# Performance work log

Measured on AMD Instinct MI355X. Metric: run time of the kernel, lower is better.

Reference implementation:

```python
import jax, jax.numpy as jnp
import numpy as np

B, N, M, L, H = 32, 4096, 256, 128, 4
GAMMA = 2.0


def setup_inputs() -> dict:
    key = jax.random.key(0)
    kx, km, kv, ku, kw = jax.random.split(key, 5)
    x = jax.random.normal(kx, (B, N, M), dtype=jnp.float32)
    masks = (jax.random.uniform(km, (B, N)) > 0.3).astype(jnp.float32)
    # VarianceScaling(scale=0.1, fan_in, uniform) ~ small init; exact dist doesn't affect math
    V = jax.random.normal(kv, (H, M, L), dtype=jnp.float32) * 0.02
    U = jax.random.normal(ku, (H, M, L), dtype=jnp.float32) * 0.02
    w = jax.random.normal(kw, (H, L, 1), dtype=jnp.float32) * 0.05
    return {"x": x, "masks": masks, "V": V, "U": U, "w": w}


def reference(x, masks, V, U, w):
    # x: [B,N,M], masks: [B,N], V/U: [H,M,L], w: [H,L,1]
    m = masks[:, None, :, None]  # [B,1,N,1] broadcast over heads
    gated = jnp.tanh(jnp.einsum('bnm,hml->bhnl', x, V)) * jax.nn.sigmoid(
        jnp.einsum('bnm,hml->bhnl', x, U))          # [B,H,N,L]
    logits = jnp.einsum('bhnl,hl->bhn', gated, w[..., 0])[..., None]  # [B,H,N,1]
    a = m * logits                                   # masked logits (as in original)
    a = m * jnp.exp(a)                               # masked exp
    a = a / jnp.sum(a, axis=2, keepdims=True)        # softmax over instances
    ag = a ** GAMMA
    a = ag / jnp.sum(ag, axis=2, keepdims=True)      # gamma-power renorm
    emb = jnp.einsum('bhnk,bnm->bhm', a, x)          # weighted sum; k is the trailing 1
    emb = emb.reshape(B, H * M)                      # concat heads along axis=1
    att = jnp.transpose(a, (1, 0, 2, 3))             # [H,B,N,1] (per-head attention list)
    return (att, emb)
```

## Files before the change

### kernel.cpp

```cpp
#include <hip/hip_runtime.h>
#include <hip/hip_bf16.h>
#include <stdint.h>

#define B_ 32
#define N_ 4096
#define M_ 256
#define L_ 128
#define H_ 4
#define BN_ (B_ * N_)

typedef __bf16 bf16x8 __attribute__((ext_vector_type(8)));
typedef float  f32x4  __attribute__((ext_vector_type(4)));

__device__ __forceinline__ unsigned short f2bf(float f) {
    unsigned int u = __float_as_uint(f);
    u += 0x7fffu + ((u >> 16) & 1u);
    return (unsigned short)(u >> 16);
}
__device__ __forceinline__ unsigned int pack2(float lo, float hi) {
    return (unsigned int)f2bf(lo) | ((unsigned int)f2bf(hi) << 16);
}

__device__ __forceinline__ void gload16(const void* g, void* l) {
    __builtin_amdgcn_global_load_lds(
        (const __attribute__((address_space(1))) unsigned int*)g,
        (__attribute__((address_space(3))) unsigned int*)l, 16, 0, 0);
}


__global__ void prep_x(const float* __restrict__ x, unsigned short* __restrict__ xb) {
    const int blk  = blockIdx.x;
    const int tile = blk >> 2, ks = blk & 3;
    const int i    = threadIdx.x;
    const int kk   = (i & 7) * 8;
    const int tl   = kk >> 5;
    const int kl   = kk & 31;
    char* dst = (char*)xb + ((size_t)tile * 8 + ks * 2 + tl) * 8192;
#pragma unroll
    for (int rep = 0; rep < 4; ++rep) {
        int row = rep * 32 + (i >> 3);
        const float* gx = x + (size_t)(tile * 128 + row) * M_ + ks * 64 + kk;
        float4 a = *(const float4*)gx;
        float4 b = *(const float4*)(gx + 4);
        uint4 o;
        o.x = pack2(a.x, a.y); o.y = pack2(a.z, a.w);
        o.z = pack2(b.x, b.y); o.w = pack2(b.z, b.w);
        int byte = (row * 64 + kl * 2) ^ ((row & 6) << 3);
        *(uint4*)(dst + byte) = o;
    }
}

__global__ void prep_vu_img(const float* __restrict__ V, const float* __restrict__ U,
                            unsigned short* __restrict__ vu) {
    __shared__ float slab[64][129];
    const int b   = blockIdx.x;
    const int mat = b & 1, ks = (b >> 1) & 3, h = b >> 3;
    const float* src = (mat ? U : V) + ((size_t)h * M_ + ks * 64) * L_;
    const int tid = threadIdx.x;
#pragma unroll
    for (int rep = 0; rep < 32; ++rep) {
        int idx = rep * 256 + tid;
        slab[idx >> 7][idx & 127] = src[(size_t)(idx >> 7) * L_ + (idx & 127)];
    }
    __syncthreads();
#pragma unroll
    for (int rep = 0; rep < 4; ++rep) {
        int cidx = rep * 256 + tid;
        int l  = cidx >> 3;
        int kk = (cidx & 7) * 8;
        uint4 o;
        o.x = pack2(slab[kk + 0][l], slab[kk + 1][l]);
        o.y = pack2(slab[kk + 2][l], slab[kk + 3][l]);
        o.z = pack2(slab[kk + 4][l], slab[kk + 5][l]);
        o.w = pack2(slab[kk + 6][l], slab[kk + 7][l]);
        int tl = kk >> 5, kl = kk & 31;
        char* dst = (char*)vu + (((size_t)(h * 8 + ks * 2 + tl)) * 2 + mat) * 8192;
        int byte = (l * 64 + kl * 2) ^ ((l & 6) << 3);
        *(uint4*)(dst + byte) = o;
    }
}

__global__ __launch_bounds__(256, 3)
void gemm_fast5(const unsigned short* __restrict__ xb,
                const unsigned short* __restrict__ vu,
                const float* __restrict__ w,
                float* __restrict__ logits) {
    __shared__ __align__(16) unsigned short xs[2][4096];
    __shared__ __align__(16) unsigned short vs[2][4096];
    __shared__ __align__(16) unsigned short us[2][4096];

    const int orig    = blockIdx.x;
    const int logical = (orig & 7) * 512 + (orig >> 3);
    const int tile    = logical >> 2;
    const int h       = logical & 3;

    const int tid  = threadIdx.x;
    const int lane = tid & 63;
    const int wv   = tid >> 6;
    const int g    = lane >> 4;
    const int c    = lane & 15;

    f32x4 accV[2][8], accU[2][8];
#pragma unroll
    for (int rf = 0; rf < 2; ++rf)
#pragma unroll
        for (int cf = 0; cf < 8; ++cf) {
            accV[rf][cf] = (f32x4){0.f, 0.f, 0.f, 0.f};
            accU[rf][cf] = (f32x4){0.f, 0.f, 0.f, 0.f};
        }

    const int soff = wv * 2048;

    const char* gxs = (const char*)xb + (size_t)tile * 65536 + soff + lane * 16;
    const char* gvs = (const char*)vu + (size_t)h * 131072 + soff + lane * 16;
    const char* gus = gvs + 8192;

    int ar = wv * 32 + c;
    const int aoff0 = (ar * 64 + g * 16) ^ ((ar & 6) << 3);
    const int aoff1 = ((ar + 16) * 64 + g * 16) ^ (((ar + 16) & 6) << 3);
    int boff[8];
#pragma unroll
    for (int cf = 0; cf < 8; ++cf) {
        int l = cf * 16 + c;
        boff[cf] = (l * 64 + g * 16) ^ ((l & 6) << 3);
    }

#define SCHED __builtin_amdgcn_sched_barrier(0)

#define STAGE(t, bufi) do {                                          \
        const char* _gx = gxs + (t) * 8192;                          \
        const char* _gv = gvs + (t) * 16384;                         \
        const char* _gu = gus + (t) * 16384;                         \
        gload16(_gx,        (char*)xs[bufi] + soff);                 \
        gload16(_gx + 1024, (char*)xs[bufi] + soff + 1024);          \
        gload16(_gv,        (char*)vs[bufi] + soff);                 \
        gload16(_gv + 1024, (char*)vs[bufi] + soff + 1024);          \
        gload16(_gu,        (char*)us[bufi] + soff);                 \
        gload16(_gu + 1024, (char*)us[bufi] + soff + 1024);          \
    } while (0)

    STAGE(0, 0);
    SCHED;

#pragma unroll
    for (int t = 0; t < 8; ++t) {
        asm volatile("s_waitcnt vmcnt(0)" ::: "memory");
        __builtin_amdgcn_s_barrier();
        SCHED;

        if (t < 7) STAGE(t + 1, (t + 1) & 1);
        SCHED;

        const int buf = t & 1;
        const char* xbuf = (const char*)xs[buf];
        const char* vbuf = (const char*)vs[buf];
        const char* ubuf = (const char*)us[buf];

        bf16x8 a0 = *(const bf16x8*)(xbuf + aoff0);
        bf16x8 a1 = *(const bf16x8*)(xbuf + aoff1);
        __builtin_amdgcn_s_setprio(1);
#pragma unroll
        for (int cf = 0; cf < 8; ++cf) {
            bf16x8 bv = *(const bf16x8*)(vbuf + boff[cf]);
            bf16x8 bu = *(const bf16x8*)(ubuf + boff[cf]);
            accV[0][cf] = __builtin_amdgcn_mfma_f32_16x16x32_bf16(a0, bv, accV[0][cf], 0, 0, 0);
            accV[1][cf] = __builtin_amdgcn_mfma_f32_16x16x32_bf16(a1, bv, accV[1][cf], 0, 0, 0);
            accU[0][cf] = __builtin_amdgcn_mfma_f32_16x16x32_bf16(a0, bu, accU[0][cf], 0, 0, 0);
            accU[1][cf] = __builtin_amdgcn_mfma_f32_16x16x32_bf16(a1, bu, accU[1][cf], 0, 0, 0);
        }
        __builtin_amdgcn_s_setprio(0);
    }
#undef STAGE
#undef SCHED

    const float* wrow = w + h * L_;
#pragma unroll
    for (int rf = 0; rf < 2; ++rf) {
        float plog[4] = {0.f, 0.f, 0.f, 0.f};
#pragma unroll
        for (int cf = 0; cf < 8; ++cf) {
            float wvv = wrow[cf * 16 + c];
#pragma unroll
            for (int i = 0; i < 4; ++i) {
                float vv = accV[rf][cf][i];
                float uu = accU[rf][cf][i];
                vv = fminf(fmaxf(vv, -20.f), 20.f);
                float A = __expf(2.f * vv);
                float E = __expf(fminf(-uu, 30.f));
                float gg = __fdividef(A - 1.f, (A + 1.f) * (1.f + E));
                plog[i] += gg * wvv;
            }
        }
#pragma unroll
        for (int i = 0; i < 4; ++i) {
            float v = plog[i];
            v += __shfl_xor(v, 1);
            v += __shfl_xor(v, 2);
            v += __shfl_xor(v, 4);
            v += __shfl_xor(v, 8);
            if (c == 0) {
                int rowflat = tile * 128 + wv * 32 + rf * 16 + g * 4 + i;
                int b = rowflat >> 12;
                int n = rowflat & (N_ - 1);
                logits[((size_t)b * H_ + h) * N_ + n] = v;
            }
        }
    }
}

__global__ void prep_vu_slow(const float* __restrict__ V, const float* __restrict__ U,
                             unsigned short* __restrict__ Vt, unsigned short* __restrict__ Ut) {
    int idx = blockIdx.x * 256 + threadIdx.x;
    int m = idx & (M_ - 1);
    int l = (idx >> 8) & (L_ - 1);
    int h = idx >> 15;
    Vt[idx] = f2bf(V[((size_t)h * M_ + m) * L_ + l]);
    Ut[idx] = f2bf(U[((size_t)h * M_ + m) * L_ + l]);
}

#define BM 128
#define BK 64

__global__ __launch_bounds__(256, 2)
void gemm_logits(const float* __restrict__ x,
                 const unsigned short* __restrict__ Vt,
                 const unsigned short* __restrict__ Ut,
                 const float* __restrict__ w,
                 float* __restrict__ logits) {
    __shared__ __align__(16) unsigned short xs[BM * BK];
    __shared__ __align__(16) unsigned short vs[L_ * BK];
    __shared__ __align__(16) unsigned short us[L_ * BK];
    __shared__ float wl[L_];

    const int h    = blockIdx.x >> 10;
    const int tile = blockIdx.x & 1023;
    const int row0 = tile * BM;
    const int tid  = threadIdx.x;
    const int lane = tid & 63;
    const int wave = tid >> 6;

    if (tid < L_) wl[tid] = w[h * L_ + tid];

    f32x4 accV[2][8], accU[2][8];
#pragma unroll
    for (int rf = 0; rf < 2; ++rf)
#pragma unroll
        for (int cf = 0; cf < 8; ++cf) {
            accV[rf][cf] = (f32x4){0.f, 0.f, 0.f, 0.f};
            accU[rf][cf] = (f32x4){0.f, 0.f, 0.f, 0.f};
        }

    const unsigned short* Vh = Vt + (size_t)h * L_ * M_;
    const unsigned short* Uh = Ut + (size_t)h * L_ * M_;
    const int g = lane >> 4;
    const int c = lane & 15;

    for (int ks = 0; ks < 4; ++ks) {
        const int k0 = ks * BK;
        __syncthreads();
#pragma unroll
        for (int p = 0; p < 4; ++p) {
            int row = p * 32 + (tid >> 3);
            int kk  = (tid & 7) * 8;
            const float* gx = x + (size_t)(row0 + row) * M_ + k0 + kk;
            float4 a = *(const float4*)gx;
            float4 b = *(const float4*)(gx + 4);
            uint4 o;
            o.x = pack2(a.x, a.y); o.y = pack2(a.z, a.w);
            o.z = pack2(b.x, b.y); o.w = pack2(b.z, b.w);
            int byte = (row * BK + kk) * 2;
            byte ^= (row & 7) << 4;
            *(uint4*)((char*)xs + byte) = o;
        }
#pragma unroll
        for (int p = 0; p < 4; ++p) {
            int l  = p * 32 + (tid >> 3);
            int kk = (tid & 7) * 8;
            uint4 v = *(const uint4*)(Vh + (size_t)l * M_ + k0 + kk);
            uint4 u = *(const uint4*)(Uh + (size_t)l * M_ + k0 + kk);
            int byte = (l * BK + kk) * 2;
            byte ^= (l & 7) << 4;
            *(uint4*)((char*)vs + byte) = v;
            *(uint4*)((char*)us + byte) = u;
        }
        __syncthreads();
#pragma unroll
        for (int ksub = 0; ksub < 2; ++ksub) {
            bf16x8 afr[2];
#pragma unroll
            for (int rf = 0; rf < 2; ++rf) {
                int row = wave * 32 + rf * 16 + c;
                int byte = (row * BK + ksub * 32 + g * 8) * 2;
                byte ^= (row & 7) << 4;
                afr[rf] = *(const bf16x8*)((const char*)xs + byte);
            }
#pragma unroll
            for (int cf = 0; cf < 8; ++cf) {
                int l = cf * 16 + c;
                int byte = (l * BK + ksub * 32 + g * 8) * 2;
                byte ^= (l & 7) << 4;
                bf16x8 bv = *(const bf16x8*)((const char*)vs + byte);
                bf16x8 bu = *(const bf16x8*)((const char*)us + byte);
#pragma unroll
                for (int rf = 0; rf < 2; ++rf) {
                    accV[rf][cf] = __builtin_amdgcn_mfma_f32_16x16x32_bf16(afr[rf], bv, accV[rf][cf], 0, 0, 0);
                    accU[rf][cf] = __builtin_amdgcn_mfma_f32_16x16x32_bf16(afr[rf], bu, accU[rf][cf], 0, 0, 0);
                }
            }
        }
    }
#pragma unroll
    for (int rf = 0; rf < 2; ++rf) {
        float plog[4] = {0.f, 0.f, 0.f, 0.f};
#pragma unroll
        for (int cf = 0; cf < 8; ++cf) {
            float wvv = wl[cf * 16 + c];
#pragma unroll
            for (int i = 0; i < 4; ++i) {
                float vv = accV[rf][cf][i];
                float uu = accU[rf][cf][i];
                vv = fminf(fmaxf(vv, -20.f), 20.f);
                float e2v = __expf(2.f * vv);
                float t = __fdividef(e2v - 1.f, e2v + 1.f);
                float s = __fdividef(1.f, 1.f + __expf(-uu));
                plog[i] += t * s * wvv;
            }
        }
#pragma unroll
        for (int i = 0; i < 4; ++i) {
            float v = plog[i];
            v += __shfl_xor(v, 1);
            v += __shfl_xor(v, 2);
            v += __shfl_xor(v, 4);
            v += __shfl_xor(v, 8);
            if (c == 0) {
                int rowflat = row0 + wave * 32 + rf * 16 + g * 4 + i;
                int b = rowflat >> 12;
                int n = rowflat & (N_ - 1);
                logits[((size_t)b * H_ + h) * N_ + n] = v;
            }
        }
    }
}

__global__ __launch_bounds__(256)
void softmax_att(const float* __restrict__ logits, const float* __restrict__ masks,
                 float* __restrict__ att) {
    const int bh = blockIdx.x;
    const int b = bh >> 2, h = bh & 3;
    __shared__ float e2s[N_];
    __shared__ float red[4];
    const int tid = threadIdx.x;

    float sum = 0.f;
#pragma unroll
    for (int i = 0; i < N_ / 256; ++i) {
        int n = i * 256 + tid;
        float lg = logits[((size_t)b * H_ + h) * N_ + n];
        float mv = masks[(size_t)b * N_ + n];
        float e = mv * __expf(mv * lg);
        float e2 = e * e;
        e2s[n] = e2;
        sum += e2;
    }
#pragma unroll
    for (int off = 32; off >= 1; off >>= 1) sum += __shfl_xor(sum, off);
    if ((tid & 63) == 0) red[tid >> 6] = sum;
    __syncthreads();
    float S = red[0] + red[1] + red[2] + red[3];
    float inv = 1.f / S;
#pragma unroll
    for (int i = 0; i < N_ / 256; ++i) {
        int n = i * 256 + tid;
        att[((size_t)h * B_ + b) * N_ + n] = e2s[n] * inv;
    }
}

#define NCH 32
#define CHUNK (N_ / NCH)

__global__ __launch_bounds__(256)
void emb_partial(const float* __restrict__ x, const float* __restrict__ att,
                 float* __restrict__ part) {
    const int bc = blockIdx.x;
    const int b = bc >> 5, ch = bc & 31;
    __shared__ float as[H_][CHUNK];
    const int tid = threadIdx.x;

    for (int i = tid; i < H_ * CHUNK; i += 256) {
        int hh = i >> 7;
        int j  = i & (CHUNK - 1);
        as[hh][j] = att[((size_t)hh * B_ + b) * N_ + ch * CHUNK + j];
    }
    __syncthreads();

    float a0 = 0.f, a1 = 0.f, a2 = 0.f, a3 = 0.f;
    const float* xp = x + ((size_t)b * N_ + ch * CHUNK) * M_ + tid;
#pragma unroll 4
    for (int j = 0; j < CHUNK; ++j) {
        float xv = xp[(size_t)j * M_];
        a0 += as[0][j] * xv;
        a1 += as[1][j] * xv;
        a2 += as[2][j] * xv;
        a3 += as[3][j] * xv;
    }
    float* pp = part + (size_t)bc * H_ * M_ + tid;
    pp[0 * M_] = a0; pp[1 * M_] = a1; pp[2 * M_] = a2; pp[3 * M_] = a3;
}

__global__ __launch_bounds__(256)
void emb_reduce(const float* __restrict__ part, float* __restrict__ emb) {
    int idx = blockIdx.x * 256 + threadIdx.x;
    int b = idx >> 10;
    int r = idx & 1023;
    float s = 0.f;
#pragma unroll
    for (int ci = 0; ci < NCH; ++ci)
        s += part[((size_t)(b * NCH + ci)) * (H_ * M_) + r];
    emb[idx] = s;
}

extern "C" void kernel_launch(void* const* d_in, const int* in_sizes, int n_in,
                              void* d_out, int out_size, void* d_ws, size_t ws_size,
                              hipStream_t stream) {
    const float* x     = (const float*)d_in[0];
    const float* masks = (const float*)d_in[1];
    const float* V     = (const float*)d_in[2];
    const float* U     = (const float*)d_in[3];
    const float* w     = (const float*)d_in[4];

    float* att = (float*)d_out;
    float* emb = att + (size_t)H_ * B_ * N_;

    char* ws = (char*)d_ws;
    const size_t XB_BYTES  = (size_t)1024 * 8 * 8192;
    const size_t VU_BYTES  = (size_t)64 * 8192;
    const size_t LG_BYTES  = (size_t)B_ * H_ * N_ * 4;
    const size_t PT_BYTES  = (size_t)B_ * NCH * H_ * M_ * 4;
    const size_t NEED_FAST = XB_BYTES + VU_BYTES + LG_BYTES + PT_BYTES;

    float* logits;
    float* partp;

    if (ws_size >= NEED_FAST) {
        unsigned short* xb = (unsigned short*)ws;
        unsigned short* vuimg = (unsigned short*)(ws + XB_BYTES);
        logits = (float*)(ws + XB_BYTES + VU_BYTES);
        partp  = (float*)(ws + XB_BYTES + VU_BYTES + LG_BYTES);

        prep_x     <<<4096, 256, 0, stream>>>(x, xb);
        prep_vu_img<<<32,   256, 0, stream>>>(V, U, vuimg);
        gemm_fast5 <<<4096, 256, 0, stream>>>(xb, vuimg, w, logits);
    } else {
        unsigned short* Vt = (unsigned short*)ws;
        unsigned short* Ut = (unsigned short*)(ws + 262144);
        logits = (float*)(ws + 524288);
        partp  = (float*)(ws + 524288 + LG_BYTES);

        prep_vu_slow<<<512, 256, 0, stream>>>(V, U, Vt, Ut);
        gemm_logits <<<4096, 256, 0, stream>>>(x, Vt, Ut, w, logits);
    }

    softmax_att<<<B_ * H_,              256, 0, stream>>>(logits, masks, att);
    emb_partial<<<B_ * NCH,             256, 0, stream>>>(x, att, partp);
    emb_reduce <<<(B_ * H_ * M_) / 256, 256, 0, stream>>>(partp, emb);
}
```

Measured before the change: 181.1 us.

## Split GEMM waves into 2x2 row/column grid and widen LDS swizzle

Each wave now computes a 64x64 quadrant (4 row fragments by 4 column fragments) instead of 32 rows by all 128 columns. This balances A and B LDS fragment loads per MFMA, cutting LDS read traffic per wave. Partial logits from the two column halves are combined through a small shared array with an extra barrier. The XOR swizzle is widened from (row&6) to (row&14) in both prep kernels and the GEMM to reduce LDS bank conflicts under the new access pattern.

```diff
diff --git a/kernel.cpp b/kernel.cpp
--- a/kernel.cpp
+++ b/kernel.cpp
@@ -45,7 +45,7 @@
         uint4 o;
         o.x = pack2(a.x, a.y); o.y = pack2(a.z, a.w);
         o.z = pack2(b.x, b.y); o.w = pack2(b.z, b.w);
-        int byte = (row * 64 + kl * 2) ^ ((row & 6) << 3);
+        int byte = (row * 64 + kl * 2) ^ ((row & 14) << 3);
         *(uint4*)(dst + byte) = o;
     }
 }
@@ -75,19 +75,20 @@
         o.w = pack2(slab[kk + 6][l], slab[kk + 7][l]);
         int tl = kk >> 5, kl = kk & 31;
         char* dst = (char*)vu + (((size_t)(h * 8 + ks * 2 + tl)) * 2 + mat) * 8192;
-        int byte = (l * 64 + kl * 2) ^ ((l & 6) << 3);
+        int byte = (l * 64 + kl * 2) ^ ((l & 14) << 3);
         *(uint4*)(dst + byte) = o;
     }
 }
 
 __global__ __launch_bounds__(256, 3)
-void gemm_fast5(const unsigned short* __restrict__ xb,
+void gemm_fast6(const unsigned short* __restrict__ xb,
                 const unsigned short* __restrict__ vu,
                 const float* __restrict__ w,
                 float* __restrict__ logits) {
     __shared__ __align__(16) unsigned short xs[2][4096];
     __shared__ __align__(16) unsigned short vs[2][4096];
     __shared__ __align__(16) unsigned short us[2][4096];
+    __shared__ float part[2][128];
 
     const int orig    = blockIdx.x;
     const int logical = (orig & 7) * 512 + (orig >> 3);
@@ -99,12 +100,14 @@
     const int wv   = tid >> 6;
     const int g    = lane >> 4;
     const int c    = lane & 15;
-
-    f32x4 accV[2][8], accU[2][8];
-#pragma unroll
-    for (int rf = 0; rf < 2; ++rf)
-#pragma unroll
-        for (int cf = 0; cf < 8; ++cf) {
+    const int wr   = wv & 1;
+    const int wc   = wv >> 1;
+
+    f32x4 accV[4][4], accU[4][4];
+#pragma unroll
+    for (int rf = 0; rf < 4; ++rf)
+#pragma unroll
+        for (int cf = 0; cf < 4; ++cf) {
             accV[rf][cf] = (f32x4){0.f, 0.f, 0.f, 0.f};
             accU[rf][cf] = (f32x4){0.f, 0.f, 0.f, 0.f};
         }
@@ -115,14 +118,16 @@
     const char* gvs = (const char*)vu + (size_t)h * 131072 + soff + lane * 16;
     const char* gus = gvs + 8192;
 
-    int ar = wv * 32 + c;
-    const int aoff0 = (ar * 64 + g * 16) ^ ((ar & 6) << 3);
-    const int aoff1 = ((ar + 16) * 64 + g * 16) ^ (((ar + 16) & 6) << 3);
-    int boff[8];
-#pragma unroll
-    for (int cf = 0; cf < 8; ++cf) {
-        int l = cf * 16 + c;
-        boff[cf] = (l * 64 + g * 16) ^ ((l & 6) << 3);
+    int aoff[4], boff[4];
+#pragma unroll
+    for (int rf = 0; rf < 4; ++rf) {
+        int r = wr * 64 + rf * 16 + c;
+        aoff[rf] = (r * 64 + g * 16) ^ ((r & 14) << 3);
+    }
+#pragma unroll
+    for (int cf = 0; cf < 4; ++cf) {
+        int l = wc * 64 + cf * 16 + c;
+        boff[cf] = (l * 64 + g * 16) ^ ((l & 14) << 3);
     }
 
 #define SCHED __builtin_amdgcn_sched_barrier(0)
@@ -156,29 +161,35 @@
         const char* vbuf = (const char*)vs[buf];
         const char* ubuf = (const char*)us[buf];
 
-        bf16x8 a0 = *(const bf16x8*)(xbuf + aoff0);
-        bf16x8 a1 = *(const bf16x8*)(xbuf + aoff1);
+        bf16x8 a0 = *(const bf16x8*)(xbuf + aoff[0]);
+        bf16x8 a1 = *(const bf16x8*)(xbuf + aoff[1]);
+        bf16x8 a2 = *(const bf16x8*)(xbuf + aoff[2]);
+        bf16x8 a3 = *(const bf16x8*)(xbuf + aoff[3]);
         __builtin_amdgcn_s_setprio(1);
 #pragma unroll
-        for (int cf = 0; cf < 8; ++cf) {
+        for (int cf = 0; cf < 4; ++cf) {
             bf16x8 bv = *(const bf16x8*)(vbuf + boff[cf]);
             bf16x8 bu = *(const bf16x8*)(ubuf + boff[cf]);
             accV[0][cf] = __builtin_amdgcn_mfma_f32_16x16x32_bf16(a0, bv, accV[0][cf], 0, 0, 0);
             accV[1][cf] = __builtin_amdgcn_mfma_f32_16x16x32_bf16(a1, bv, accV[1][cf], 0, 0, 0);
+            accV[2][cf] = __builtin_amdgcn_mfma_f32_16x16x32_bf16(a2, bv, accV[2][cf], 0, 0, 0);
+            accV[3][cf] = __builtin_amdgcn_mfma_f32_16x16x32_bf16(a3, bv, accV[3][cf], 0, 0, 0);
             accU[0][cf] = __builtin_amdgcn_mfma_f32_16x16x32_bf16(a0, bu, accU[0][cf], 0, 0, 0);
             accU[1][cf] = __builtin_amdgcn_mfma_f32_16x16x32_bf16(a1, bu, accU[1][cf], 0, 0, 0);
+            accU[2][cf] = __builtin_amdgcn_mfma_f32_16x16x32_bf16(a2, bu, accU[2][cf], 0, 0, 0);
+            accU[3][cf] = __builtin_amdgcn_mfma_f32_16x16x32_bf16(a3, bu, accU[3][cf], 0, 0, 0);
         }
         __builtin_amdgcn_s_setprio(0);
     }
 #undef STAGE
 #undef SCHED
 
-    const float* wrow = w + h * L_;
-#pragma unroll
-    for (int rf = 0; rf < 2; ++rf) {
+    const float* wrow = w + h * L_ + wc * 64;
+#pragma unroll
+    for (int rf = 0; rf < 4; ++rf) {
         float plog[4] = {0.f, 0.f, 0.f, 0.f};
 #pragma unroll
-        for (int cf = 0; cf < 8; ++cf) {
+        for (int cf = 0; cf < 4; ++cf) {
             float wvv = wrow[cf * 16 + c];
 #pragma unroll
             for (int i = 0; i < 4; ++i) {
@@ -198,13 +209,17 @@
             v += __shfl_xor(v, 2);
             v += __shfl_xor(v, 4);
             v += __shfl_xor(v, 8);
-            if (c == 0) {
-                int rowflat = tile * 128 + wv * 32 + rf * 16 + g * 4 + i;
-                int b = rowflat >> 12;
-                int n = rowflat & (N_ - 1);
-                logits[((size_t)b * H_ + h) * N_ + n] = v;
-            }
-        }
+            if (c == 0)
+                part[wc][wr * 64 + rf * 16 + g * 4 + i] = v;
+        }
+    }
+    __syncthreads();
+    if (tid < 128) {
+        float v = part[0][tid] + part[1][tid];
+        int rowflat = tile * 128 + tid;
+        int b = rowflat >> 12;
+        int n = rowflat & (N_ - 1);
+        logits[((size_t)b * H_ + h) * N_ + n] = v;
     }
 }
 
@@ -450,7 +465,7 @@
 
         prep_x     <<<4096, 256, 0, stream>>>(x, xb);
         prep_vu_img<<<32,   256, 0, stream>>>(V, U, vuimg);
-        gemm_fast5 <<<4096, 256, 0, stream>>>(xb, vuimg, w, logits);
+        gemm_fast6 <<<4096, 256, 0, stream>>>(xb, vuimg, w, logits);
     } else {
         unsigned short* Vt = (unsigned short*)ws;
         unsigned short* Ut = (unsigned short*)(ws + 262144);
```

New measurement: 174.0 us. 3.9% less time.
